# Optimization experiments

Measured on AMD Instinct MI355X. Metric: run time of the kernel, lower is better.

The kernel has to match this reference:

```python
import jax, jax.numpy as jnp
import numpy as np

B, T, IN_DIM, D, H, F, L = 16, 64, 128, 512, 8, 2048, 4  # T == DATA_ROUNDS_PER_GAME
HD = D // H
SCALE = 1.0 / np.sqrt(HD)
NEG = -1e9


def setup_inputs() -> dict:
    key = jax.random.key(0)
    ks = jax.random.split(key, 10)
    s = lambda k, shape, fan: (jax.random.normal(k, shape, jnp.float32) * (fan ** -0.5)).astype(jnp.float32)
    return {
        "x": jax.random.normal(ks[0], (B, T, IN_DIM), jnp.float32),
        "fc_w": s(ks[1], (IN_DIM, D), IN_DIM), "fc_b": jnp.zeros((D,), jnp.float32),
        "w_qkv": s(ks[2], (L, D, 3 * D), D), "b_qkv": jnp.zeros((L, 3 * D), jnp.float32),
        "w_o": s(ks[3], (L, D, D), D), "b_o": jnp.zeros((L, D), jnp.float32),
        "ln1_g": jnp.ones((L, D), jnp.float32), "ln1_b": jnp.zeros((L, D), jnp.float32),
        "w_ff1": s(ks[4], (L, D, F), D), "b_ff1": jnp.zeros((L, F), jnp.float32),
        "w_ff2": s(ks[5], (L, F, D), F), "b_ff2": jnp.zeros((L, D), jnp.float32),
        "ln2_g": jnp.ones((L, D), jnp.float32), "ln2_b": jnp.zeros((L, D), jnp.float32),
        "cls_w1": s(ks[6], (D, D // 2), D), "cls_b1": jnp.zeros((D // 2,), jnp.float32),
        "cls_w2": s(ks[7], (D // 2, 2), D // 2), "cls_b2": jnp.zeros((2,), jnp.float32),
    }


def _ln(x, g, b, eps=1e-5):
    m = x.mean(-1, keepdims=True)
    v = ((x - m) ** 2).mean(-1, keepdims=True)
    return (x - m) * jax.lax.rsqrt(v + eps) * g + b


def _encoder(h, bias, w_qkv, b_qkv, w_o, b_o, ln1_g, ln1_b, w_ff1, b_ff1, w_ff2, b_ff2, ln2_g, ln2_b):
    # post-norm TransformerEncoderLayer (PyTorch default), dropout=0
    for l in range(L):
        Bh, Th = h.shape[0], h.shape[1]
        qkv = h @ w_qkv[l] + b_qkv[l]                      # [B,T,3D]
        q, k, v = jnp.split(qkv, 3, axis=-1)
        q = q.reshape(Bh, Th, H, HD)
        k = k.reshape(Bh, Th, H, HD)
        v = v.reshape(Bh, Th, H, HD)
        scores = jnp.einsum('bqhd,bkhd->bhqk', q, k) * SCALE + bias
        attn = jax.nn.softmax(scores, axis=-1)
        o = jnp.einsum('bhqk,bkhd->bqhd', attn, v).reshape(Bh, Th, D)
        h = _ln(h + o @ w_o[l] + b_o[l], ln1_g[l], ln1_b[l])
        ff = jax.nn.relu(h @ w_ff1[l] + b_ff1[l]) @ w_ff2[l] + b_ff2[l]
        h = _ln(h + ff, ln2_g[l], ln2_b[l])
    return h


def reference(x, fc_w, fc_b, w_qkv, b_qkv, w_o, b_o, ln1_g, ln1_b, w_ff1, b_ff1,
              w_ff2, b_ff2, ln2_g, ln2_b, cls_w1, cls_b1, cls_w2, cls_b2):
    h0 = jax.nn.relu(x @ fc_w + fc_b)                       # [B,T,D]

    def per_prefix(i):
        # keys restricted to positions <= i reproduces re-running the encoder
        # on the prefix x[:, :i+1]; we read position i (the prefix's last token).
        keep = jnp.arange(T) <= i
        bias = jnp.where(keep, 0.0, NEG).astype(h0.dtype)[None, None, None, :]  # [1,1,1,T]
        out = _encoder(h0, bias, w_qkv, b_qkv, w_o, b_o, ln1_g, ln1_b,
                       w_ff1, b_ff1, w_ff2, b_ff2, ln2_g, ln2_b)
        return jnp.take(out, i, axis=1)                     # [B,D]

    y = jax.vmap(per_prefix)(jnp.arange(T))                 # [T,B,D]
    y = jnp.transpose(y, (1, 0, 2))                         # [B,T,D]
    z = jax.nn.relu(y @ cls_w1 + cls_b1) @ cls_w2 + cls_b2  # [B,T,2]
    return jax.nn.log_softmax(z, axis=-1)
```

## Files before the change

kernel.cpp:

```cpp
#include <hip/hip_runtime.h>
#include <math.h>

using u16 = unsigned short;
using u32 = unsigned int;

constexpr int Bc = 16;
constexpr int Tc = 64;
constexpr int INc = 128;
constexpr int Dc = 512;
constexpr int Hc = 8;
constexpr int Fc = 2048;
constexpr int Lc = 4;
constexpr float SCALEc = 0.125f;

constexpr int NGc = 3;
constexpr int g_p0[NGc]   = {0, 35, 51};
constexpr int g_np[NGc]   = {35, 16, 13};
constexpr int g_start[NGc]= {0, 12160, 24192};
constexpr int g_M[NGc]    = {12288, 12032, 12672};
constexpr int g_M3[NGc]   = {640, 256, 256};
constexpr int g_doff[NGc] = {0, 560, 816};
constexpr int GMAXc = 12672;
constexpr int DALLc = 1024;
constexpr int DPADc = 1152;
constexpr int VTSc  = GMAXc + 64;

typedef __attribute__((ext_vector_type(8))) short bf16x8;
typedef __attribute__((ext_vector_type(4))) float f32x4;

__device__ __forceinline__ int rowbase(int p) {
  const int q = p >> 3, r = p & 7;
  return 128 * (4 * q * (q + 1) + r * (q + 1));
}

__device__ __forceinline__ float bf2f(u16 u) {
  union { u32 i; float f; } c; c.i = (u32)u << 16; return c.f;
}
__device__ __forceinline__ u16 f2bf(float f) {
  union { float f; u32 u; } c{f};
  u32 r = (c.u + 0x7fffu + ((c.u >> 16) & 1u)) >> 16;
  return (u16)r;
}

template<bool RELU>
__global__ __launch_bounds__(256) void gemm_kernel(
    const float* __restrict__ A, const float* __restrict__ W,
    const float* __restrict__ bias, float* __restrict__ C,
    u16* __restrict__ Cb, int M, int K, int N)
{
  __shared__ float As[128][17];
  __shared__ float Ws[16][64];
  const int tid = threadIdx.x;
  const int tx = tid & 15, ty = tid >> 4;
  const int row0 = blockIdx.y * 128, col0 = blockIdx.x * 64;
  float acc[8][4];
#pragma unroll
  for (int i = 0; i < 8; ++i)
#pragma unroll
    for (int j = 0; j < 4; ++j) acc[i][j] = 0.f;
  const int ar = tid >> 1, ak = (tid & 1) * 8;
  const int wr = tid >> 4, wc = (tid & 15) * 4;
  for (int k0 = 0; k0 < K; k0 += 16) {
    const float* ap = A + (size_t)(row0 + ar) * K + k0 + ak;
    float4 a0 = *(const float4*)ap;
    float4 a1 = *(const float4*)(ap + 4);
    As[ar][ak+0]=a0.x; As[ar][ak+1]=a0.y; As[ar][ak+2]=a0.z; As[ar][ak+3]=a0.w;
    As[ar][ak+4]=a1.x; As[ar][ak+5]=a1.y; As[ar][ak+6]=a1.z; As[ar][ak+7]=a1.w;
    *(float4*)&Ws[wr][wc] = *(const float4*)(W + (size_t)(k0 + wr) * N + col0 + wc);
    __syncthreads();
#pragma unroll
    for (int kk = 0; kk < 16; ++kk) {
      const float4 w4 = *(const float4*)&Ws[kk][tx * 4];
#pragma unroll
      for (int i = 0; i < 8; ++i) {
        const float av = As[ty + 16 * i][kk];
        acc[i][0] += av * w4.x; acc[i][1] += av * w4.y;
        acc[i][2] += av * w4.z; acc[i][3] += av * w4.w;
      }
    }
    __syncthreads();
  }
#pragma unroll
  for (int i = 0; i < 8; ++i) {
    const int r = row0 + ty + 16 * i, c = col0 + tx * 4;
    float4 v;
    v.x = acc[i][0] + bias[c+0]; v.y = acc[i][1] + bias[c+1];
    v.z = acc[i][2] + bias[c+2]; v.w = acc[i][3] + bias[c+3];
    if (RELU) { v.x=fmaxf(v.x,0.f); v.y=fmaxf(v.y,0.f); v.z=fmaxf(v.z,0.f); v.w=fmaxf(v.w,0.f); }
    *(float4*)&C[(size_t)r * N + c] = v;
    uint2 pk;
    pk.x = (u32)f2bf(v.x) | ((u32)f2bf(v.y) << 16);
    pk.y = (u32)f2bf(v.z) | ((u32)f2bf(v.w) << 16);
    *(uint2*)&Cb[(size_t)r * N + c] = pk;
  }
}

__global__ __launch_bounds__(256) void transpose_conv(
    const float* __restrict__ src, u16* __restrict__ dst, int K, int N)
{
  __shared__ float t[32][33];
  const int bx = blockIdx.x * 32;
  const int by = blockIdx.y * 32;
  const int x = threadIdx.x, y = threadIdx.y;
#pragma unroll
  for (int i = 0; i < 32; i += 8) t[y + i][x] = src[(size_t)(by + y + i) * N + bx + x];
  __syncthreads();
#pragma unroll
  for (int i = 0; i < 32; i += 8)
    dst[(size_t)(bx + y + i) * K + by + x] = f2bf(t[x][y + i]);
}

__global__ __launch_bounds__(256) void transpose_v(
    const u16* __restrict__ qkvsrc, u16* __restrict__ vt, int vstride)
{
  __shared__ u16 t[64][65];
  const int r0 = blockIdx.x * 64;
  const int d0 = blockIdx.y * 64;
  const int tid = threadIdx.x;
  const int rr = tid >> 2, cc = (tid & 3) * 16;
  const u16* src = qkvsrc + (size_t)(r0 + rr) * 1536 + 1024 + d0 + cc;
  union { uint4 v; u16 s[8]; } ua, ub;
  ua.v = *(const uint4*)src;
  ub.v = *(const uint4*)(src + 8);
#pragma unroll
  for (int i = 0; i < 8; ++i) { t[rr][cc + i] = ua.s[i]; t[rr][cc + 8 + i] = ub.s[i]; }
  __syncthreads();
  const int dd = tid >> 2, kk = (tid & 3) * 16;
  union { uint4 v; u16 s[8]; } w0, w1;
#pragma unroll
  for (int i = 0; i < 8; ++i) { w0.s[i] = t[kk + i][dd]; w1.s[i] = t[kk + 8 + i][dd]; }
  u16* dst = vt + (size_t)(d0 + dd) * vstride + r0 + kk;
  *(uint4*)dst = w0.v;
  *(uint4*)(dst + 8) = w1.v;
}

__device__ __forceinline__ void stage_tile(const u16* __restrict__ src, int ldk, u16* lds)
{
  const int tid = threadIdx.x;
#pragma unroll
  for (int q = 0; q < 4; ++q) {
    const int p16 = tid + (q << 8);
    const int row = p16 >> 3;
    const int s   = p16 & 7;
    const int k16 = s ^ (row & 7);
    const u16* g = src + (size_t)row * ldk + (k16 << 3);
    __builtin_amdgcn_global_load_lds(
        (const __attribute__((address_space(1))) void*)g,
        (__attribute__((address_space(3))) void*)(lds + (p16 << 3)),
        16, 0, 0);
  }
}

template<bool RELU, bool OUT_BF16>
__global__ __launch_bounds__(256) void gemm_mfma(
    const u16* __restrict__ A, const u16* __restrict__ Wt,
    const float* __restrict__ bias, void* __restrict__ Cout,
    int M, int K, int N)
{
  __shared__ u16 As[2][128 * 64];
  __shared__ u16 Bs[2][128 * 64];

  const int tid  = threadIdx.x;
  const int lane = tid & 63;
  const int wave = tid >> 6;
  const int wr = wave >> 1;
  const int wc = wave & 1;

  const int gx = gridDim.x;
  const int nwg = gx * gridDim.y;
  const int lin = blockIdx.y * gx + blockIdx.x;
  const int qq = nwg >> 3, r8 = nwg & 7;
  const int xcd = lin & 7, pos = lin >> 3;
  const int orig = (xcd < r8) ? (xcd * (qq + 1) + pos)
                              : (r8 * (qq + 1) + (xcd - r8) * qq + pos);
  const int row0 = (orig / gx) * 128;
  const int col0 = (orig % gx) * 128;

  f32x4 acc[4][4];
#pragma unroll
  for (int i = 0; i < 4; ++i)
#pragma unroll
    for (int j = 0; j < 4; ++j) acc[i][j] = f32x4{0.f, 0.f, 0.f, 0.f};

  const int nk = K >> 6;
  const int arow = wr * 64 + (lane & 15);
  const int brow = wc * 64 + (lane & 15);
  const int kq   = lane >> 4;

  stage_tile(A  + (size_t)row0 * K, K, &As[0][0]);
  stage_tile(Wt + (size_t)col0 * K, K, &Bs[0][0]);

  for (int t = 0; t < nk; ++t) {
    const int cur = t & 1;
    if (t + 1 < nk) {
      const int k0 = (t + 1) << 6;
      stage_tile(A  + (size_t)row0 * K + k0, K, &As[cur ^ 1][0]);
      stage_tile(Wt + (size_t)col0 * K + k0, K, &Bs[cur ^ 1][0]);
      asm volatile("s_waitcnt vmcnt(8)\n\ts_barrier" ::: "memory");
    } else {
      asm volatile("s_waitcnt vmcnt(0)\n\ts_barrier" ::: "memory");
    }
    const u16* Ab = &As[cur][0];
    const u16* Bb = &Bs[cur][0];
#pragma unroll
    for (int kk = 0; kk < 2; ++kk) {
      bf16x8 af[4], bfr[4];
      const int c = kk * 4 + kq;
#pragma unroll
      for (int i = 0; i < 4; ++i) {
        const int ra = arow + i * 16;
        af[i]  = *reinterpret_cast<const bf16x8*>(Ab + ra * 64 + ((c ^ (ra & 7)) << 3));
        const int rb = brow + i * 16;
        bfr[i] = *reinterpret_cast<const bf16x8*>(Bb + rb * 64 + ((c ^ (rb & 7)) << 3));
      }
#pragma unroll
      for (int mi = 0; mi < 4; ++mi)
#pragma unroll
        for (int ni = 0; ni < 4; ++ni)
          acc[mi][ni] = __builtin_amdgcn_mfma_f32_16x16x32_bf16(af[mi], bfr[ni], acc[mi][ni], 0, 0, 0);
    }
    asm volatile("s_barrier" ::: "memory");
  }

  const int r0 = row0 + wr * 64 + ((lane >> 4) << 2);
  const int c0 = col0 + wc * 64 + (lane & 15);
#pragma unroll
  for (int mi = 0; mi < 4; ++mi)
#pragma unroll
    for (int ni = 0; ni < 4; ++ni) {
      const int col = c0 + ni * 16;
      const float bsv = bias[col];
#pragma unroll
      for (int j = 0; j < 4; ++j) {
        const int row = r0 + mi * 16 + j;
        float o = acc[mi][ni][j] + bsv;
        if (RELU) o = fmaxf(o, 0.f);
        if (OUT_BF16) ((u16*)Cout)[(size_t)row * N + col] = f2bf(o);
        else          ((float*)Cout)[(size_t)row * N + col] = o;
      }
    }
}

template<bool SHARED>
__global__ __launch_bounds__(64) void attn_mfma_kernel(
    const u16* __restrict__ qkv, const u16* __restrict__ vt, int vstride,
    u16* __restrict__ attno, int p0, int gstart)
{
  const int hh = blockIdx.x, b = blockIdx.y, p = p0 + blockIdx.z;
  const int NT = p + 1;
  const int NT8 = (NT + 7) & ~7;
  const int rb = rowbase(p) + b * NT8 - gstart;
  const int sb = SHARED ? (b * 64) : rb;
  const int tid = threadIdx.x;
  const int lc = tid & 15, lg = tid >> 4;

  __shared__ u16 Plds[64][72];
  __shared__ u16 VTl[4096];
  __shared__ float invl[64];

  {
    const u16* vbase = vt + (size_t)(hh * 64) * vstride + sb;
#pragma unroll
    for (int it = 0; it < 8; ++it) {
      const int gi = tid + (it << 6);
      const int dd = gi >> 3, s = gi & 7;
      const u16* src = vbase + (size_t)dd * vstride + ((s ^ (dd & 7)) << 3);
      __builtin_amdgcn_global_load_lds(
          (const __attribute__((address_space(1))) void*)src,
          (__attribute__((address_space(3))) void*)(&VTl[gi << 3]), 16, 0, 0);
    }
  }

  f32x4 st[4][4];
#pragma unroll
  for (int i = 0; i < 4; ++i)
#pragma unroll
    for (int j = 0; j < 4; ++j) st[i][j] = f32x4{0.f, 0.f, 0.f, 0.f};

#pragma unroll
  for (int kt = 0; kt < 2; ++kt) {
    bf16x8 kf[4], qf[4];
#pragma unroll
    for (int t = 0; t < 4; ++t) {
      if (t * 16 < NT) {
        const size_t rbase = (size_t)(sb + t * 16 + lc) * 1536 + hh * 64 + kt * 32 + lg * 8;
        qf[t] = *reinterpret_cast<const bf16x8*>(qkv + rbase);
        kf[t] = *reinterpret_cast<const bf16x8*>(qkv + rbase + 512);
      }
    }
#pragma unroll
    for (int mi = 0; mi < 4; ++mi)
      if (mi * 16 < NT)
#pragma unroll
        for (int ni = 0; ni < 4; ++ni)
          if (ni * 16 < NT)
            st[mi][ni] = __builtin_amdgcn_mfma_f32_16x16x32_bf16(kf[mi], qf[ni], st[mi][ni], 0, 0, 0);
  }

#pragma unroll
  for (int ni = 0; ni < 4; ++ni) {
    float mm = -3.0e38f;
#pragma unroll
    for (int mi = 0; mi < 4; ++mi)
#pragma unroll
      for (int e = 0; e < 4; ++e)
        if (16 * mi + 4 * lg + e < NT) mm = fmaxf(mm, st[mi][ni][e]);
    mm = fmaxf(mm, __shfl_xor(mm, 16));
    mm = fmaxf(mm, __shfl_xor(mm, 32));
    float ss = 0.f;
#pragma unroll
    for (int mi = 0; mi < 4; ++mi) {
      u16 pb[4];
#pragma unroll
      for (int e = 0; e < 4; ++e) {
        const float pe = (16 * mi + 4 * lg + e < NT)
                           ? __expf((st[mi][ni][e] - mm) * SCALEc) : 0.f;
        ss += pe;
        pb[e] = f2bf(pe);
      }
      uint2 pk;
      pk.x = (u32)pb[0] | ((u32)pb[1] << 16);
      pk.y = (u32)pb[2] | ((u32)pb[3] << 16);
      *reinterpret_cast<uint2*>(&Plds[16 * ni + lc][16 * mi + 4 * lg]) = pk;
    }
    ss += __shfl_xor(ss, 16);
    ss += __shfl_xor(ss, 32);
    if (lg == 0) invl[16 * ni + lc] = 1.f / ss;
  }

  asm volatile("s_waitcnt vmcnt(0)" ::: "memory");
  __syncthreads();

  f32x4 oc[4][4];
#pragma unroll
  for (int i = 0; i < 4; ++i)
#pragma unroll
    for (int j = 0; j < 4; ++j) oc[i][j] = f32x4{0.f, 0.f, 0.f, 0.f};

#pragma unroll
  for (int kt = 0; kt < 2; ++kt) {
    if (kt * 32 < NT) {
      bf16x8 pa[4], vbf[4];
#pragma unroll
      for (int t = 0; t < 4; ++t) {
        if (t * 16 < NT)
          pa[t] = *reinterpret_cast<const bf16x8*>(&Plds[t * 16 + lc][kt * 32 + lg * 8]);
        const int dd = t * 16 + lc;
        vbf[t] = *reinterpret_cast<const bf16x8*>(
            &VTl[dd * 64 + (((4 * kt + lg) ^ (lc & 7)) << 3)]);
      }
#pragma unroll
      for (int qt = 0; qt < 4; ++qt)
        if (qt * 16 < NT)
#pragma unroll
          for (int dt = 0; dt < 4; ++dt)
            oc[qt][dt] = __builtin_amdgcn_mfma_f32_16x16x32_bf16(pa[qt], vbf[dt], oc[qt][dt], 0, 0, 0);
    }
  }

#pragma unroll
  for (int qt = 0; qt < 4; ++qt) {
    if (qt * 16 < NT) {
#pragma unroll
      for (int e = 0; e < 4; ++e) {
        const int qrow = qt * 16 + 4 * lg + e;
        if (qrow < NT) {
          const float inv = invl[qrow];
          u16* dst = attno + (size_t)(rb + qrow) * Dc + hh * 64 + lc;
#pragma unroll
          for (int dt = 0; dt < 4; ++dt)
            dst[dt * 16] = f2bf(oc[qt][dt][e] * inv);
        }
      }
    }
  }
}

__global__ __launch_bounds__(64) void attn_diag_kernel(
    const u16* __restrict__ kv3, const u16* __restrict__ qd,
    u16* __restrict__ attno_d, int p0, int gstart, int doff)
{
  const int hh = blockIdx.x, b = blockIdx.y, pl = blockIdx.z;
  const int p = p0 + pl;
  const int NT = p + 1;
  const int NT8 = (NT + 7) & ~7;
  const int rb = rowbase(p) + b * NT8 - gstart;
  const int tid = threadIdx.x;
  const int rd = doff + pl * 16 + b;

  __shared__ u16 Ks[64][64];
  __shared__ u16 Vs[64][64];

  const int lrow = tid >> 3;
  const int lc8  = tid & 7;
  for (int t0 = 0; t0 < NT; t0 += 8) {
    const int tr = rb + t0 + lrow;
    const int csrc = (lc8 ^ lrow) << 3;
    const u16* gk = kv3 + (size_t)tr * 1024 + hh * 64 + csrc;
    const u16* gv = kv3 + (size_t)tr * 1024 + 512 + hh * 64 + csrc;
    __builtin_amdgcn_global_load_lds(
        (const __attribute__((address_space(1))) void*)gk,
        (__attribute__((address_space(3))) void*)(&Ks[t0][0] + tid * 8), 16, 0, 0);
    __builtin_amdgcn_global_load_lds(
        (const __attribute__((address_space(1))) void*)gv,
        (__attribute__((address_space(3))) void*)(&Vs[t0][0] + tid * 8), 16, 0, 0);
  }

  const u16* qp = qd + (size_t)rd * Dc + hh * 64;
  float qv[64];
#pragma unroll
  for (int c8 = 0; c8 < 8; ++c8) {
    const bf16x8 q8 = *reinterpret_cast<const bf16x8*>(qp + c8 * 8);
#pragma unroll
    for (int i = 0; i < 8; ++i) qv[c8 * 8 + i] = bf2f((u16)q8[i]);
  }
  asm volatile("s_waitcnt vmcnt(0)" ::: "memory");
  __syncthreads();

  float dot = -1e30f;
  if (tid < NT) {
    dot = 0.f;
#pragma unroll
    for (int c8 = 0; c8 < 8; ++c8) {
      const bf16x8 k8 = *reinterpret_cast<const bf16x8*>(
          &Ks[tid][0] + ((c8 ^ (tid & 7)) << 3));
#pragma unroll
      for (int i = 0; i < 8; ++i) dot += qv[c8 * 8 + i] * bf2f((u16)k8[i]);
    }
    dot *= SCALEc;
  }
  float mm = dot;
#pragma unroll
  for (int off = 32; off; off >>= 1) mm = fmaxf(mm, __shfl_xor(mm, off));
  const float pt = __expf(dot - mm);
  float s = pt;
#pragma unroll
  for (int off = 32; off; off >>= 1) s += __shfl_xor(s, off);
  const float inv = 1.f / s;

  float o = 0.f;
  for (int t = 0; t < NT; ++t) {
    const float ptt = __shfl(pt, t);
    o += ptt * bf2f(Vs[t][(((tid >> 3) ^ (t & 7)) << 3) + (tid & 7)]);
  }
  attno_d[(size_t)rd * Dc + hh * 64 + tid] = f2bf(o * inv);
}

__device__ inline float wave_sum(float v) {
#pragma unroll
  for (int off = 32; off; off >>= 1) v += __shfl_xor(v, off);
  return v;
}

__global__ __launch_bounds__(256) void res_ln_kernel(
    u16* __restrict__ hb, const u16* __restrict__ tmpb,
    const float* __restrict__ g, const float* __restrict__ bt)
{
  const size_t row = (size_t)blockIdx.x * 4 + (threadIdx.x >> 6);
  const int t = threadIdx.x & 63;
  float v[8];
  float s = 0.f;
#pragma unroll
  for (int i = 0; i < 8; ++i) {
    v[i] = bf2f(hb[row * Dc + i * 64 + t]) + bf2f(tmpb[row * Dc + i * 64 + t]);
    s += v[i];
  }
  s = wave_sum(s);
  const float mean = s * (1.f / 512.f);
  float vs = 0.f;
#pragma unroll
  for (int i = 0; i < 8; ++i) { const float d = v[i] - mean; vs += d * d; }
  vs = wave_sum(vs);
  const float rstd = rsqrtf(vs * (1.f / 512.f) + 1e-5f);
#pragma unroll
  for (int i = 0; i < 8; ++i)
    hb[row * Dc + i * 64 + t] =
        f2bf((v[i] - mean) * rstd * g[i * 64 + t] + bt[i * 64 + t]);
}

__global__ __launch_bounds__(64) void res_ln0_kernel(
    const u16* __restrict__ h0b, u16* __restrict__ hb,
    const u16* __restrict__ tmpb, const float* __restrict__ g,
    const float* __restrict__ bt, int p0, int gstart)
{
  const int t = blockIdx.x, b = blockIdx.y, p = p0 + blockIdx.z;
  if (t > p) return;
  const int NT8 = (p + 8) & ~7;
  const size_t row = (size_t)(rowbase(p) + b * NT8 + t - gstart);
  const int tt = threadIdx.x;
  const u16* src = h0b + (size_t)(b * 64 + t) * Dc;
  float v[8];
  float s = 0.f;
#pragma unroll
  for (int i = 0; i < 8; ++i) {
    v[i] = bf2f(src[i * 64 + tt]) + bf2f(tmpb[row * Dc + i * 64 + tt]);
    s += v[i];
  }
  s = wave_sum(s);
  const float mean = s * (1.f / 512.f);
  float vs = 0.f;
#pragma unroll
  for (int i = 0; i < 8; ++i) { const float d = v[i] - mean; vs += d * d; }
  vs = wave_sum(vs);
  const float rstd = rsqrtf(vs * (1.f / 512.f) + 1e-5f);
#pragma unroll
  for (int i = 0; i < 8; ++i)
    hb[row * Dc + i * 64 + tt] =
        f2bf((v[i] - mean) * rstd * g[i * 64 + tt] + bt[i * 64 + tt]);
}

__global__ __launch_bounds__(128) void gather_diag(
    const u16* __restrict__ hb, u16* __restrict__ hbd,
    int p0, int gstart, int doff)
{
  const int pl = blockIdx.x >> 4, b = blockIdx.x & 15;
  const int p = p0 + pl;
  const int NT8 = (p + 8) & ~7;
  const size_t src = (size_t)(rowbase(p) + b * NT8 + p - gstart);
  ((uint2*)(hbd + (size_t)(doff + blockIdx.x) * Dc))[threadIdx.x] =
      ((const uint2*)(hb + src * Dc))[threadIdx.x];
}

__global__ __launch_bounds__(128) void scatter_out(
    const u16* __restrict__ hbd, float* __restrict__ yb, int p0, int doff)
{
  const int pl = blockIdx.x >> 4, b = blockIdx.x & 15;
  const int p = p0 + pl;
  const uint2 v = ((const uint2*)(hbd + (size_t)(doff + blockIdx.x) * Dc))[threadIdx.x];
  float4 f;
  f.x = bf2f((u16)(v.x & 0xffff)); f.y = bf2f((u16)(v.x >> 16));
  f.z = bf2f((u16)(v.y & 0xffff)); f.w = bf2f((u16)(v.y >> 16));
  ((float4*)(yb + ((size_t)(b * 64 + p)) * Dc))[threadIdx.x] = f;
}

__global__ __launch_bounds__(256) void cls_kernel(
    const float* __restrict__ y, const float* __restrict__ w1, const float* __restrict__ b1,
    const float* __restrict__ w2, const float* __restrict__ b2, float* __restrict__ out)
{
  const int row = blockIdx.x;
  const int j = threadIdx.x;
  __shared__ float ys[512];
  ys[j]       = y[(size_t)row * Dc + j];
  ys[j + 256] = y[(size_t)row * Dc + 256 + j];
  __syncthreads();

  float acc = b1[j];
  for (int d = 0; d < 512; ++d) acc += ys[d] * w1[(size_t)d * 256 + j];
  acc = fmaxf(acc, 0.f);

  float c0 = acc * w2[j * 2 + 0];
  float c1 = acc * w2[j * 2 + 1];
  c0 = wave_sum(c0);
  c1 = wave_sum(c1);

  __shared__ float r0[4], r1[4];
  const int w = j >> 6, lane = j & 63;
  if (lane == 0) { r0[w] = c0; r1[w] = c1; }
  __syncthreads();
  if (j == 0) {
    const float z0 = r0[0] + r0[1] + r0[2] + r0[3] + b2[0];
    const float z1 = r1[0] + r1[1] + r1[2] + r1[3] + b2[1];
    const float mz = fmaxf(z0, z1);
    const float lse = mz + logf(expf(z0 - mz) + expf(z1 - mz));
    out[row * 2 + 0] = z0 - lse;
    out[row * 2 + 1] = z1 - lse;
  }
}

extern "C" void kernel_launch(void* const* d_in, const int* in_sizes, int n_in,
                              void* d_out, int out_size, void* d_ws, size_t ws_size,
                              hipStream_t stream)
{
  if (n_in < 19) return;
  const float* x      = (const float*)d_in[0];
  const float* fc_w   = (const float*)d_in[1];
  const float* fc_b   = (const float*)d_in[2];
  const float* w_qkv  = (const float*)d_in[3];
  const float* b_qkv  = (const float*)d_in[4];
  const float* w_o    = (const float*)d_in[5];
  const float* b_o    = (const float*)d_in[6];
  const float* ln1_g  = (const float*)d_in[7];
  const float* ln1_b  = (const float*)d_in[8];
  const float* w_ff1  = (const float*)d_in[9];
  const float* b_ff1  = (const float*)d_in[10];
  const float* w_ff2  = (const float*)d_in[11];
  const float* b_ff2  = (const float*)d_in[12];
  const float* ln2_g  = (const float*)d_in[13];
  const float* ln2_b  = (const float*)d_in[14];
  const float* cls_w1 = (const float*)d_in[15];
  const float* cls_b1 = (const float*)d_in[16];
  const float* cls_w2 = (const float*)d_in[17];
  const float* cls_b2 = (const float*)d_in[18];
  float* out = (float*)d_out;

  char* wp = (char*)d_ws;
  auto alloc = [&](size_t bytes) -> char* {
    char* p = wp; wp += (bytes + 255) & ~(size_t)255; return p;
  };
  float* h0  = (float*)alloc((size_t)Bc * Tc * Dc * 4);
  u16*   h0b = (u16*)  alloc((size_t)Bc * Tc * Dc * 2);
  float* yb  = (float*)alloc((size_t)Bc * Tc * Dc * 4);
  u16*   qkv0= (u16*)  alloc((size_t)Bc * Tc * 3 * Dc * 2);
  u16*   vt0 = (u16*)  alloc((size_t)Dc * Bc * Tc * 2);
  u16 *wtq[Lc], *wto[Lc], *wtf1[Lc], *wtf2[Lc];
  for (int l = 0; l < Lc; ++l) {
    wtq[l]  = (u16*)alloc((size_t)3 * Dc * Dc * 2);
    wto[l]  = (u16*)alloc((size_t)Dc * Dc * 2);
    wtf1[l] = (u16*)alloc((size_t)Fc * Dc * 2);
    wtf2[l] = (u16*)alloc((size_t)Dc * Fc * 2);
  }
  const size_t RS = (size_t)GMAXc + 64;
  u16*   hb    = (u16*)  alloc((size_t)GMAXc * Dc * 2);
  u16*   qkvb  = (u16*)  alloc(RS * 3 * Dc * 2);
  u16*   attno = (u16*)  alloc((size_t)GMAXc * Dc * 2);
  u16*   tmpb  = (u16*)  alloc((size_t)GMAXc * Dc * 2);
  u16*   ffb   = (u16*)  alloc((size_t)GMAXc * Fc * 2);
  u16*   vt    = (u16*)  alloc((size_t)Dc * VTSc * 2);
  u16*   hbdiag= (u16*)  alloc((size_t)DPADc * Dc * 2);
  u16*   attnd = (u16*)  alloc((size_t)DPADc * Dc * 2);
  u16*   qd    = (u16*)  alloc((size_t)DPADc * Dc * 2);
  if ((size_t)(wp - (char*)d_ws) > ws_size) return;
  u16* kv3 = qkvb;

  const dim3 tb(32, 8);
  for (int l = 0; l < Lc; ++l) {
    transpose_conv<<<dim3(3 * Dc / 32, Dc / 32), tb, 0, stream>>>(
        w_qkv + (size_t)l * Dc * 3 * Dc, wtq[l], Dc, 3 * Dc);
    transpose_conv<<<dim3(Dc / 32, Dc / 32), tb, 0, stream>>>(
        w_o + (size_t)l * Dc * Dc, wto[l], Dc, Dc);
    transpose_conv<<<dim3(Fc / 32, Dc / 32), tb, 0, stream>>>(
        w_ff1 + (size_t)l * Dc * Fc, wtf1[l], Dc, Fc);
    transpose_conv<<<dim3(Dc / 32, Fc / 32), tb, 0, stream>>>(
        w_ff2 + (size_t)l * Fc * Dc, wtf2[l], Fc, Dc);
  }

  gemm_kernel<true><<<dim3(Dc / 64, (Bc * Tc) / 128), 256, 0, stream>>>(
      x, fc_w, fc_b, h0, h0b, Bc * Tc, INc, Dc);

  gemm_mfma<false, true><<<dim3(3 * Dc / 128, (Bc * Tc) / 128), 256, 0, stream>>>(
      h0b, wtq[0], b_qkv, qkv0, Bc * Tc, Dc, 3 * Dc);
  transpose_v<<<dim3((Bc * Tc) / 64, 8), 256, 0, stream>>>(qkv0, vt0, Bc * Tc);

  for (int g = 0; g < NGc; ++g) {
    const int p0 = g_p0[g], np = g_np[g], gs = g_start[g], Mg = g_M[g];
    const int M3 = g_M3[g], doff = g_doff[g];

    attn_mfma_kernel<true><<<dim3(Hc, Bc, np), 64, 0, stream>>>(
        qkv0, vt0, Bc * Tc, attno, p0, gs);
    gemm_mfma<false, true><<<dim3(Dc / 128, Mg / 128), 256, 0, stream>>>(
        attno, wto[0], b_o, tmpb, Mg, Dc, Dc);
    res_ln0_kernel<<<dim3(64, 16, np), 64, 0, stream>>>(
        h0b, hb, tmpb, ln1_g, ln1_b, p0, gs);
    gemm_mfma<true, true><<<dim3(Fc / 128, Mg / 128), 256, 0, stream>>>(
        hb, wtf1[0], b_ff1, ffb, Mg, Dc, Fc);
    gemm_mfma<false, true><<<dim3(Dc / 128, Mg / 128), 256, 0, stream>>>(
        ffb, wtf2[0], b_ff2, tmpb, Mg, Fc, Dc);
    res_ln_kernel<<<Mg / 4, 256, 0, stream>>>(hb, tmpb, ln2_g, ln2_b);

    for (int l = 1; l < 3; ++l) {
      gemm_mfma<false, true><<<dim3(3 * Dc / 128, Mg / 128), 256, 0, stream>>>(
          hb, wtq[l], b_qkv + (size_t)l * 3 * Dc, qkvb, Mg, Dc, 3 * Dc);
      transpose_v<<<dim3(Mg / 64, 8), 256, 0, stream>>>(qkvb, vt, VTSc);
      attn_mfma_kernel<false><<<dim3(Hc, Bc, np), 64, 0, stream>>>(
          qkvb, vt, VTSc, attno, p0, gs);
      gemm_mfma<false, true><<<dim3(Dc / 128, Mg / 128), 256, 0, stream>>>(
          attno, wto[l], b_o + (size_t)l * Dc, tmpb, Mg, Dc, Dc);
      res_ln_kernel<<<Mg / 4, 256, 0, stream>>>(hb, tmpb, ln1_g + l * Dc, ln1_b + l * Dc);
      gemm_mfma<true, true><<<dim3(Fc / 128, Mg / 128), 256, 0, stream>>>(
          hb, wtf1[l], b_ff1 + (size_t)l * Fc, ffb, Mg, Dc, Fc);
      gemm_mfma<false, true><<<dim3(Dc / 128, Mg / 128), 256, 0, stream>>>(
          ffb, wtf2[l], b_ff2 + (size_t)l * Dc, tmpb, Mg, Fc, Dc);
      res_ln_kernel<<<Mg / 4, 256, 0, stream>>>(hb, tmpb, ln2_g + l * Dc, ln2_b + l * Dc);
    }

    {
      const int l = 3;
      gather_diag<<<np * 16, 128, 0, stream>>>(hb, hbdiag, p0, gs, doff);
      gemm_mfma<false, true><<<dim3(Dc / 128, M3 / 128), 256, 0, stream>>>(
          hbdiag + (size_t)doff * Dc, wtq[l], b_qkv + (size_t)l * 3 * Dc,
          qd + (size_t)doff * Dc, M3, Dc, Dc);
      gemm_mfma<false, true><<<dim3(2 * Dc / 128, Mg / 128), 256, 0, stream>>>(
          hb, wtq[l] + (size_t)512 * Dc, b_qkv + (size_t)l * 3 * Dc + 512,
          kv3, Mg, Dc, 2 * Dc);
      attn_diag_kernel<<<dim3(Hc, Bc, np), 64, 0, stream>>>(
          kv3, qd, attnd, p0, gs, doff);
    }
  }

  {
    const int l = 3;
    gemm_mfma<false, true><<<dim3(Dc / 128, DALLc / 128), 256, 0, stream>>>(
        attnd, wto[l], b_o + (size_t)l * Dc, tmpb, DALLc, Dc, Dc);
    res_ln_kernel<<<DALLc / 4, 256, 0, stream>>>(hbdiag, tmpb,
                                                 ln1_g + l * Dc, ln1_b + l * Dc);
    gemm_mfma<true, true><<<dim3(Fc / 128, DALLc / 128), 256, 0, stream>>>(
        hbdiag, wtf1[l], b_ff1 + (size_t)l * Fc, ffb, DALLc, Dc, Fc);
    gemm_mfma<false, true><<<dim3(Dc / 128, DALLc / 128), 256, 0, stream>>>(
        ffb, wtf2[l], b_ff2 + (size_t)l * Dc, tmpb, DALLc, Fc, Dc);
    res_ln_kernel<<<DALLc / 4, 256, 0, stream>>>(hbdiag, tmpb,
                                                 ln2_g + l * Dc, ln2_b + l * Dc);
    for (int g = 0; g < NGc; ++g)
      scatter_out<<<g_np[g] * 16, 128, 0, stream>>>(hbdiag, yb, g_p0[g], g_doff[g]);
  }

  cls_kernel<<<Bc * Tc, 256, 0, stream>>>(yb, cls_w1, cls_b1, cls_w2, cls_b2, out);
}
```

Before: 1.601 ms.

## Process prefixes in two larger groups and read diag output directly in classifier

Measured after the change: 1.599 ms. No clear change (-0.2%).

```diff
diff --git a/kernel.cpp b/kernel.cpp
--- a/kernel.cpp
+++ b/kernel.cpp
@@ -13,14 +13,14 @@
 constexpr int Lc = 4;
 constexpr float SCALEc = 0.125f;
 
-constexpr int NGc = 3;
-constexpr int g_p0[NGc]   = {0, 35, 51};
-constexpr int g_np[NGc]   = {35, 16, 13};
-constexpr int g_start[NGc]= {0, 12160, 24192};
-constexpr int g_M[NGc]    = {12288, 12032, 12672};
-constexpr int g_M3[NGc]   = {640, 256, 256};
-constexpr int g_doff[NGc] = {0, 560, 816};
-constexpr int GMAXc = 12672;
+constexpr int NGc = 2;
+constexpr int g_p0[NGc]   = {0, 44};
+constexpr int g_np[NGc]   = {44, 20};
+constexpr int g_start[NGc]= {0, 18432};
+constexpr int g_M[NGc]    = {18432, 18432};
+constexpr int g_M3[NGc]   = {768, 384};
+constexpr int g_doff[NGc] = {0, 704};
+constexpr int GMAXc = 18432;
 constexpr int DALLc = 1024;
 constexpr int DPADc = 1152;
 constexpr int VTSc  = GMAXc + 64;
@@ -521,27 +521,18 @@
       ((const uint2*)(hb + src * Dc))[threadIdx.x];
 }
 
-__global__ __launch_bounds__(128) void scatter_out(
-    const u16* __restrict__ hbd, float* __restrict__ yb, int p0, int doff)
-{
-  const int pl = blockIdx.x >> 4, b = blockIdx.x & 15;
-  const int p = p0 + pl;
-  const uint2 v = ((const uint2*)(hbd + (size_t)(doff + blockIdx.x) * Dc))[threadIdx.x];
-  float4 f;
-  f.x = bf2f((u16)(v.x & 0xffff)); f.y = bf2f((u16)(v.x >> 16));
-  f.z = bf2f((u16)(v.y & 0xffff)); f.w = bf2f((u16)(v.y >> 16));
-  ((float4*)(yb + ((size_t)(b * 64 + p)) * Dc))[threadIdx.x] = f;
-}
-
 __global__ __launch_bounds__(256) void cls_kernel(
-    const float* __restrict__ y, const float* __restrict__ w1, const float* __restrict__ b1,
-    const float* __restrict__ w2, const float* __restrict__ b2, float* __restrict__ out)
+    const u16* __restrict__ hbd, const float* __restrict__ w1,
+    const float* __restrict__ b1, const float* __restrict__ w2,
+    const float* __restrict__ b2, float* __restrict__ out)
 {
   const int row = blockIdx.x;
+  const int b = row >> 6, p = row & 63;
+  const int rd = (p < 44) ? (p * 16 + b) : (704 + (p - 44) * 16 + b);
   const int j = threadIdx.x;
   __shared__ float ys[512];
-  ys[j]       = y[(size_t)row * Dc + j];
-  ys[j + 256] = y[(size_t)row * Dc + 256 + j];
+  ys[j]       = bf2f(hbd[(size_t)rd * Dc + j]);
+  ys[j + 256] = bf2f(hbd[(size_t)rd * Dc + 256 + j]);
   __syncthreads();
 
   float acc = b1[j];
@@ -599,7 +590,6 @@
   };
   float* h0  = (float*)alloc((size_t)Bc * Tc * Dc * 4);
   u16*   h0b = (u16*)  alloc((size_t)Bc * Tc * Dc * 2);
-  float* yb  = (float*)alloc((size_t)Bc * Tc * Dc * 4);
   u16*   qkv0= (u16*)  alloc((size_t)Bc * Tc * 3 * Dc * 2);
   u16*   vt0 = (u16*)  alloc((size_t)Dc * Bc * Tc * 2);
   u16 *wtq[Lc], *wto[Lc], *wtf1[Lc], *wtf2[Lc];
@@ -699,9 +689,7 @@
         ffb, wtf2[l], b_ff2 + (size_t)l * Dc, tmpb, DALLc, Fc, Dc);
     res_ln_kernel<<<DALLc / 4, 256, 0, stream>>>(hbdiag, tmpb,
                                                  ln2_g + l * Dc, ln2_b + l * Dc);
-    for (int g = 0; g < NGc; ++g)
-      scatter_out<<<g_np[g] * 16, 128, 0, stream>>>(hbdiag, yb, g_p0[g], g_doff[g]);
-  }
-
-  cls_kernel<<<Bc * Tc, 256, 0, stream>>>(yb, cls_w1, cls_b1, cls_w2, cls_b2, out);
-}
+  }
+
+  cls_kernel<<<Bc * Tc, 256, 0, stream>>>(hbdiag, cls_w1, cls_b1, cls_w2, cls_b2, out);
+}
```
